# Optimization experiments

Measured on AMD Instinct MI355X. Metric: run time of the kernel, lower is better.

## Reference

```python
import jax, jax.numpy as jnp
import numpy as np


def setup_inputs() -> dict:
    key = jax.random.key(0)
    ka, kb = jax.random.split(key)
    a = jax.random.normal(ka, (8, 2048, 1024), dtype=jnp.float32)
    b = jax.random.normal(kb, (8, 2048, 1024), dtype=jnp.float32)
    return {"a": a, "b": b}


def reference(a, b):
    # e[b,i,j] = <a_i, b_j>
    e = jnp.einsum("bid,bjd->bij", a, b)  # [B, La, Lb]
    e_b = jax.nn.softmax(e, axis=2)        # softmax over b-tokens
    e_a = jax.nn.softmax(e, axis=1)        # softmax over a-tokens
    a_tilda = jnp.einsum("bij,bjd->bid", e_b, b)  # [B, La, D]
    b_tilda = jnp.einsum("bij,bid->bjd", e_a, a)  # [B, Lb, D]
    return (a_tilda, b_tilda)
```

## Files before the change

kernel.cpp:

```cpp
#include <hip/hip_runtime.h>

#define BATCH 8
#define L 2048
#define D 1024

#define PB_OFF  (L * L)
#define PAT_OFF (L * L + (L * L) / 2)
#define SLOT_F  (2 * L * L)

typedef __attribute__((ext_vector_type(8))) short bf16x8;
typedef __attribute__((ext_vector_type(4))) float f32x4;

static __device__ inline unsigned short f2bf(float x) {
  union { float f; unsigned u; } v; v.f = x;
  unsigned r = v.u + 0x7fff + ((v.u >> 16) & 1);
  return (unsigned short)(r >> 16);
}
static __device__ inline float bf2f(unsigned short h) {
  union { unsigned u; float f; } v; v.u = ((unsigned)h) << 16; return v.f;
}
static __device__ inline unsigned pack2(float x, float y) {
  return (unsigned)f2bf(x) | ((unsigned)f2bf(y) << 16);
}
static __device__ inline void split2(float x, float y, unsigned &hi, unsigned &lo) {
  unsigned short hx = f2bf(x), hy = f2bf(y);
  float rx = x - bf2f(hx), ry = y - bf2f(hy);
  hi = (unsigned)hx | ((unsigned)hy << 16);
  lo = (unsigned)f2bf(rx) | ((unsigned)f2bf(ry) << 16);
}

#define GLL16(gp, lp) __builtin_amdgcn_global_load_lds(                        \
    (const __attribute__((address_space(1))) void*)(gp),                       \
    (__attribute__((address_space(3))) void*)(lp), 16, 0, 0)

static __device__ inline void stage2(const unsigned short* __restrict__ g,
                                     size_t o0, size_t o1,
                                     unsigned short* l, int wb) {
  GLL16(g + o0, l + wb);
  GLL16(g + o1, l + wb + 2048);
}

__global__ __launch_bounds__(256) void k_prep(const float* __restrict__ A,
                                              const float* __restrict__ Bm,
                                              unsigned short* __restrict__ at,
                                              unsigned short* __restrict__ bt,
                                              unsigned short* __restrict__ ah,
                                              unsigned short* __restrict__ al,
                                              unsigned short* __restrict__ bh,
                                              unsigned short* __restrict__ bl) {
  const int z = blockIdx.z, batch = z & 7;
  const bool isA = z < 8;
  const float* src = (isA ? A : Bm) + (size_t)batch * L * D;
  unsigned short* dst = (isA ? at : bt) + (size_t)batch * D * L;
  unsigned short* ph = (isA ? ah : bh) + (size_t)batch * L * D;
  unsigned short* pl = (isA ? al : bl) + (size_t)batch * L * D;
  const int i0 = blockIdx.x * 64, d0 = blockIdx.y * 64;
  __shared__ float sT[64][65];
  const int tid = threadIdx.x;
#pragma unroll
  for (int it = 0; it < 4; ++it) {
    int idx = tid + it * 256;
    int row = idx >> 4, c4 = (idx & 15) * 4;
    float4 v = *(const float4*)(src + (size_t)(i0 + row) * D + d0 + c4);
    unsigned h0, l0, h1, l1;
    split2(v.x, v.y, h0, l0); split2(v.z, v.w, h1, l1);
    size_t po = (size_t)(i0 + row) * D + d0 + c4;
    *(uint2*)&ph[po] = make_uint2(h0, h1);
    *(uint2*)&pl[po] = make_uint2(l0, l1);
    sT[row][c4 + 0] = v.x; sT[row][c4 + 1] = v.y;
    sT[row][c4 + 2] = v.z; sT[row][c4 + 3] = v.w;
  }
  __syncthreads();
#pragma unroll
  for (int it = 0; it < 4; ++it) {
    int idx = tid + it * 256;
    int orow = idx >> 4, c4 = (idx & 15) * 4;
    uint2 o = make_uint2(pack2(sT[c4 + 0][orow], sT[c4 + 1][orow]),
                         pack2(sT[c4 + 2][orow], sT[c4 + 3][orow]));
    *(uint2*)&dst[(size_t)(d0 + orow) * L + i0 + c4] = o;
  }
}

__global__ __launch_bounds__(256) void k_gemm_e(const unsigned short* __restrict__ ah,
                                                const unsigned short* __restrict__ al,
                                                const unsigned short* __restrict__ bh,
                                                const unsigned short* __restrict__ bl,
                                                float* __restrict__ ws, int b0) {
  const int bz = blockIdx.z, batch = b0 + bz;
  const size_t po = (size_t)batch * L * D;
  float* e = ws + (size_t)bz * SLOT_F;
  const int i0 = blockIdx.x * 128, j0 = blockIdx.y * 128;
  __shared__ unsigned short sAh[128 * 32], sAl[128 * 32];
  __shared__ unsigned short sBh[128 * 32], sBl[128 * 32];
  const int tid = threadIdx.x, lane = tid & 63, wave = tid >> 6;
  const int wm = (wave & 1) * 64, wn = (wave >> 1) * 64;
  const int q = lane >> 4, lr = lane & 15;
  const int soff = wave * 1024 + lane * 16;
  const int srow = soff >> 6, scol = (soff & 63) >> 1;
  const int wb = wave * 512;
  const unsigned short* gAh = ah + po; const unsigned short* gAl = al + po;
  const unsigned short* gBh = bh + po; const unsigned short* gBl = bl + po;
  const size_t ga0 = (size_t)(i0 + srow) * D + scol, ga1 = ga0 + (size_t)64 * D;
  const size_t gb0 = (size_t)(j0 + srow) * D + scol, gb1 = gb0 + (size_t)64 * D;
  f32x4 acc[4][4] = {};
  for (int k0 = 0; k0 < D; k0 += 32) {
    __syncthreads();
    stage2(gAh, ga0 + k0, ga1 + k0, sAh, wb);
    stage2(gAl, ga0 + k0, ga1 + k0, sAl, wb);
    stage2(gBh, gb0 + k0, gb1 + k0, sBh, wb);
    stage2(gBl, gb0 + k0, gb1 + k0, sBl, wb);
    __syncthreads();
    bf16x8 fah[4], fbh[4], fx[4];
#pragma unroll
    for (int t = 0; t < 4; ++t) {
      fah[t] = *(const bf16x8*)&sAh[(wm + t * 16 + lr) * 32 + q * 8];
      fbh[t] = *(const bf16x8*)&sBh[(wn + t * 16 + lr) * 32 + q * 8];
    }
#pragma unroll
    for (int mi = 0; mi < 4; ++mi)
#pragma unroll
      for (int ni = 0; ni < 4; ++ni)
        acc[mi][ni] = __builtin_amdgcn_mfma_f32_16x16x32_bf16(fah[mi], fbh[ni], acc[mi][ni], 0, 0, 0);
#pragma unroll
    for (int t = 0; t < 4; ++t)
      fx[t] = *(const bf16x8*)&sBl[(wn + t * 16 + lr) * 32 + q * 8];
#pragma unroll
    for (int mi = 0; mi < 4; ++mi)
#pragma unroll
      for (int ni = 0; ni < 4; ++ni)
        acc[mi][ni] = __builtin_amdgcn_mfma_f32_16x16x32_bf16(fah[mi], fx[ni], acc[mi][ni], 0, 0, 0);
#pragma unroll
    for (int t = 0; t < 4; ++t)
      fx[t] = *(const bf16x8*)&sAl[(wm + t * 16 + lr) * 32 + q * 8];
#pragma unroll
    for (int mi = 0; mi < 4; ++mi)
#pragma unroll
      for (int ni = 0; ni < 4; ++ni)
        acc[mi][ni] = __builtin_amdgcn_mfma_f32_16x16x32_bf16(fx[mi], fbh[ni], acc[mi][ni], 0, 0, 0);
  }
#pragma unroll
  for (int mi = 0; mi < 4; ++mi)
#pragma unroll
    for (int ni = 0; ni < 4; ++ni)
#pragma unroll
      for (int r = 0; r < 4; ++r)
        e[(size_t)(i0 + wm + mi * 16 + q * 4 + r) * L + (j0 + wn + ni * 16 + lr)] =
            acc[mi][ni][r];
}

__global__ __launch_bounds__(256) void k_rowsoft(float* __restrict__ ws) {
  float* slot = ws + (size_t)blockIdx.y * SLOT_F;
  const int row = blockIdx.x, tid = threadIdx.x;
  const float* er = slot + (size_t)row * L;
  float v[8]; float m = -INFINITY;
#pragma unroll
  for (int r = 0; r < 8; ++r) { v[r] = er[tid + r * 256]; m = fmaxf(m, v[r]); }
  __shared__ float red[4];
#pragma unroll
  for (int o = 32; o; o >>= 1) m = fmaxf(m, __shfl_xor(m, o));
  if ((tid & 63) == 0) red[tid >> 6] = m;
  __syncthreads();
  m = fmaxf(fmaxf(red[0], red[1]), fmaxf(red[2], red[3]));
  float ex[8], s = 0.f;
#pragma unroll
  for (int r = 0; r < 8; ++r) { ex[r] = __expf(v[r] - m); s += ex[r]; }
  __syncthreads();
#pragma unroll
  for (int o = 32; o; o >>= 1) s += __shfl_xor(s, o);
  if ((tid & 63) == 0) red[tid >> 6] = s;
  __syncthreads();
  const float inv = 1.0f / (red[0] + red[1] + red[2] + red[3]);
  unsigned short* P = (unsigned short*)(slot + PB_OFF) + (size_t)row * L;
#pragma unroll
  for (int r = 0; r < 8; ++r) P[tid + r * 256] = f2bf(ex[r] * inv);
}

__global__ __launch_bounds__(512) void k_colsoft(float* __restrict__ ws) {
  float* slot = ws + (size_t)blockIdx.y * SLOT_F;
  const int j0 = blockIdx.x * 64;
  const int tid = threadIdx.x;
  const int c = tid & 63, rq = tid >> 6;
  const float* e = slot;
  const float* ec = e + j0 + c;
  float m = -INFINITY;
#pragma unroll 8
  for (int i = rq; i < L; i += 8) m = fmaxf(m, ec[(size_t)i * L]);
  __shared__ float red[8][64];
  red[rq][c] = m;
  __syncthreads();
#pragma unroll
  for (int k = 0; k < 8; ++k) m = fmaxf(m, red[k][c]);
  float s = 0.f;
#pragma unroll 8
  for (int i = rq; i < L; i += 8) s += __expf(ec[(size_t)i * L] - m);
  __syncthreads();
  red[rq][c] = s;
  __syncthreads();
  s = 0.f;
#pragma unroll
  for (int k = 0; k < 8; ++k) s += red[k][c];
  const float inv = 1.0f / s;
  __shared__ float scm[64], sci[64];
  if (rq == 0) { scm[c] = m; sci[c] = inv; }
  __shared__ unsigned short sT[64][72];
  unsigned short* PaT = (unsigned short*)(slot + PAT_OFF);
  for (int ii0 = 0; ii0 < L; ii0 += 64) {
    __syncthreads();
#pragma unroll
    for (int p = 0; p < 2; ++p) {
      int idx = tid + p * 512;
      int r = idx >> 4, c4 = (idx & 15) * 4;
      float4 v = *(const float4*)(e + (size_t)(ii0 + r) * L + j0 + c4);
      sT[c4 + 0][r] = f2bf(__expf(v.x - scm[c4 + 0]) * sci[c4 + 0]);
      sT[c4 + 1][r] = f2bf(__expf(v.y - scm[c4 + 1]) * sci[c4 + 1]);
      sT[c4 + 2][r] = f2bf(__expf(v.z - scm[c4 + 2]) * sci[c4 + 2]);
      sT[c4 + 3][r] = f2bf(__expf(v.w - scm[c4 + 3]) * sci[c4 + 3]);
    }
    __syncthreads();
    {
      int cc = tid >> 3, r8 = (tid & 7) * 8;
      uint4 o = *(const uint4*)&sT[cc][r8];
      *(uint4*)&PaT[(size_t)(j0 + cc) * L + ii0 + r8] = o;
    }
  }
}

__global__ __launch_bounds__(256) void k_pv(const unsigned short* __restrict__ Wt,
                                            const float* __restrict__ ws, int pOff,
                                            float* __restrict__ outB, int b0) {
  const int bz = blockIdx.z, batch = b0 + bz;
  const unsigned short* P = (const unsigned short*)(ws + (size_t)bz * SLOT_F + pOff);
  const unsigned short* W = Wt + (size_t)batch * D * L;
  const int m0 = blockIdx.x * 128, d0 = blockIdx.y * 128;
  __shared__ unsigned short sP[128 * 32], sW[128 * 32];
  const int tid = threadIdx.x, lane = tid & 63, wave = tid >> 6;
  const int wm = (wave & 1) * 64, wn = (wave >> 1) * 64;
  const int q = lane >> 4, lr = lane & 15;
  const int soff = wave * 1024 + lane * 16;
  const int srow = soff >> 6, scol = (soff & 63) >> 1;
  const int wb = wave * 512;
  const size_t gp0 = (size_t)(m0 + srow) * L + scol, gp1 = gp0 + (size_t)64 * L;
  const size_t gw0 = (size_t)(d0 + srow) * L + scol, gw1 = gw0 + (size_t)64 * L;
  f32x4 acc[4][4] = {};
  for (int k0 = 0; k0 < L; k0 += 32) {
    __syncthreads();
    stage2(P, gp0 + k0, gp1 + k0, sP, wb);
    stage2(W, gw0 + k0, gw1 + k0, sW, wb);
    __syncthreads();
    bf16x8 fa[4], fb[4];
#pragma unroll
    for (int t = 0; t < 4; ++t) {
      fa[t] = *(const bf16x8*)&sP[(wm + t * 16 + lr) * 32 + q * 8];
      fb[t] = *(const bf16x8*)&sW[(wn + t * 16 + lr) * 32 + q * 8];
    }
#pragma unroll
    for (int mi = 0; mi < 4; ++mi)
#pragma unroll
      for (int ni = 0; ni < 4; ++ni)
        acc[mi][ni] = __builtin_amdgcn_mfma_f32_16x16x32_bf16(fa[mi], fb[ni], acc[mi][ni], 0, 0, 0);
  }
  float* o = outB + (size_t)batch * L * D;
#pragma unroll
  for (int mi = 0; mi < 4; ++mi)
#pragma unroll
    for (int ni = 0; ni < 4; ++ni)
#pragma unroll
      for (int r = 0; r < 4; ++r)
        o[(size_t)(m0 + wm + mi * 16 + q * 4 + r) * D + (d0 + wn + ni * 16 + lr)] =
            acc[mi][ni][r];
}

extern "C" void kernel_launch(void* const* d_in, const int* in_sizes, int n_in,
                              void* d_out, int out_size, void* d_ws, size_t ws_size,
                              hipStream_t stream) {
  const float* a = (const float*)d_in[0];
  const float* b = (const float*)d_in[1];
  float* out = (float*)d_out;
  const size_t PL = (size_t)BATCH * D * L;
  unsigned short* at = (unsigned short*)d_ws;
  unsigned short* bt = at + PL;
  unsigned short* ah = bt + PL;
  unsigned short* al = ah + PL;
  unsigned short* bh = al + PL;
  unsigned short* bl = bh + PL;
  float* slots = (float*)(bl + PL);
  const size_t base_bytes = 6 * PL * sizeof(unsigned short);
  const size_t slot_bytes = (size_t)SLOT_F * sizeof(float);
  int S = 1;
  if (ws_size > base_bytes + slot_bytes)
    S = (int)((ws_size - base_bytes) / slot_bytes);
  if (S > BATCH) S = BATCH;
  if (S < 1) S = 1;

  hipLaunchKernelGGL(k_prep, dim3(L / 64, D / 64, 2 * BATCH), dim3(256), 0, stream,
                     a, b, at, bt, ah, al, bh, bl);
  for (int b0 = 0; b0 < BATCH; b0 += S) {
    int nb = (BATCH - b0 < S) ? (BATCH - b0) : S;
    hipLaunchKernelGGL(k_gemm_e, dim3(16, 16, nb), dim3(256), 0, stream,
                       ah, al, bh, bl, slots, b0);
    hipLaunchKernelGGL(k_rowsoft, dim3(L, nb), dim3(256), 0, stream, slots);
    hipLaunchKernelGGL(k_colsoft, dim3(L / 64, nb), dim3(512), 0, stream, slots);
    hipLaunchKernelGGL(k_pv, dim3(16, 8, nb), dim3(256), 0, stream,
                       bt, slots, PB_OFF, out, b0);
    hipLaunchKernelGGL(k_pv, dim3(16, 8, nb), dim3(256), 0, stream,
                       at, slots, PAT_OFF, out + (size_t)BATCH * L * D, b0);
  }
}
```

Baseline: 811.0 us.

## Fuse column-max into QK GEMM, split colsoftmax, defer normalization, merge PV launches

The QK GEMM epilogue now computes per-tile column maxima, so the column softmax no longer needs a separate max pass over E. Column work is split into small stat kernels plus a parallel exp/transposition kernel that also emits partial sums. Normalization by row and column reciprocal sums is deferred to the PV epilogue. The two PV launches are merged into one grid, with a 64-wide K tile, swizzled LDS and a GLL16 direct-load path. This adds more launches and extra stat buffers in the workspace.

Measured after the change: 738.3 us. -9.0%, faster.

```diff
diff --git a/kernel.cpp b/kernel.cpp
--- a/kernel.cpp
+++ b/kernel.cpp
@@ -6,7 +6,13 @@
 
 #define PB_OFF  (L * L)
 #define PAT_OFF (L * L + (L * L) / 2)
-#define SLOT_F  (2 * L * L)
+#define STAT    (2 * L * L)
+#define ROWINV  0
+#define CMAXP   (L)
+#define CMAX    (17 * L)
+#define CSUMP   (18 * L)
+#define CINV    (26 * L)
+#define SLOT_F  (2 * L * L + 28 * L)
 
 typedef __attribute__((ext_vector_type(8))) short bf16x8;
 typedef __attribute__((ext_vector_type(4))) float f32x4;
@@ -92,6 +98,7 @@
   const int i0 = blockIdx.x * 128, j0 = blockIdx.y * 128;
   __shared__ unsigned short sAh[128 * 32], sAl[128 * 32];
   __shared__ unsigned short sBh[128 * 32], sBl[128 * 32];
+  __shared__ float pcm[128];
   const int tid = threadIdx.x, lane = tid & 63, wave = tid >> 6;
   const int wm = (wave & 1) * 64, wn = (wave >> 1) * 64;
   const int q = lane >> 4, lr = lane & 15;
@@ -146,6 +153,29 @@
       for (int r = 0; r < 4; ++r)
         e[(size_t)(i0 + wm + mi * 16 + q * 4 + r) * L + (j0 + wn + ni * 16 + lr)] =
             acc[mi][ni][r];
+  float cmax[4];
+#pragma unroll
+  for (int ni = 0; ni < 4; ++ni) {
+    float m = acc[0][ni][0];
+#pragma unroll
+    for (int mi = 0; mi < 4; ++mi)
+#pragma unroll
+      for (int r = 0; r < 4; ++r) m = fmaxf(m, acc[mi][ni][r]);
+    m = fmaxf(m, __shfl_xor(m, 16));
+    m = fmaxf(m, __shfl_xor(m, 32));
+    cmax[ni] = m;
+  }
+  if (!(wave & 1) && q == 0)
+#pragma unroll
+    for (int ni = 0; ni < 4; ++ni) pcm[wn + ni * 16 + lr] = cmax[ni];
+  __syncthreads();
+  if ((wave & 1) && q == 0) {
+#pragma unroll
+    for (int ni = 0; ni < 4; ++ni) {
+      int c = wn + ni * 16 + lr;
+      e[STAT + CMAXP + (size_t)(i0 >> 7) * L + j0 + c] = fmaxf(cmax[ni], pcm[c]);
+    }
+  }
 }
 
 __global__ __launch_bounds__(256) void k_rowsoft(float* __restrict__ ws) {
@@ -169,105 +199,139 @@
   for (int o = 32; o; o >>= 1) s += __shfl_xor(s, o);
   if ((tid & 63) == 0) red[tid >> 6] = s;
   __syncthreads();
-  const float inv = 1.0f / (red[0] + red[1] + red[2] + red[3]);
   unsigned short* P = (unsigned short*)(slot + PB_OFF) + (size_t)row * L;
 #pragma unroll
-  for (int r = 0; r < 8; ++r) P[tid + r * 256] = f2bf(ex[r] * inv);
-}
-
-__global__ __launch_bounds__(512) void k_colsoft(float* __restrict__ ws) {
-  float* slot = ws + (size_t)blockIdx.y * SLOT_F;
-  const int j0 = blockIdx.x * 64;
+  for (int r = 0; r < 8; ++r) P[tid + r * 256] = f2bf(ex[r]);
+  if (tid == 0)
+    slot[STAT + ROWINV + row] = 1.0f / (red[0] + red[1] + red[2] + red[3]);
+}
+
+__global__ __launch_bounds__(256) void k_colstat2(float* __restrict__ ws) {
+  float* st = ws + (size_t)blockIdx.y * SLOT_F + STAT;
+  const int j = blockIdx.x * 256 + threadIdx.x;
+  float m = st[CMAXP + j];
+#pragma unroll
+  for (int k = 1; k < 16; ++k) m = fmaxf(m, st[CMAXP + (size_t)k * L + j]);
+  st[CMAX + j] = m;
+}
+
+__global__ __launch_bounds__(256) void k_colexp(float* __restrict__ ws) {
+  float* slot = ws + (size_t)blockIdx.z * SLOT_F;
+  const float* e = slot;
+  float* st = slot + STAT;
+  const int j0 = blockIdx.x * 64, i0 = blockIdx.y * 256;
   const int tid = threadIdx.x;
-  const int c = tid & 63, rq = tid >> 6;
-  const float* e = slot;
-  const float* ec = e + j0 + c;
-  float m = -INFINITY;
-#pragma unroll 8
-  for (int i = rq; i < L; i += 8) m = fmaxf(m, ec[(size_t)i * L]);
-  __shared__ float red[8][64];
-  red[rq][c] = m;
-  __syncthreads();
-#pragma unroll
-  for (int k = 0; k < 8; ++k) m = fmaxf(m, red[k][c]);
+  const int rr = tid >> 4, c4 = (tid & 15) * 4;
+  __shared__ unsigned short sT[64][72];
+  __shared__ float psumL[16][64];
+  float cm[4], ps[4] = {0.f, 0.f, 0.f, 0.f};
+#pragma unroll
+  for (int k = 0; k < 4; ++k) cm[k] = st[CMAX + j0 + c4 + k];
+  unsigned short* PaT = (unsigned short*)(slot + PAT_OFF);
+  for (int sub = 0; sub < 4; ++sub) {
+    const int ib = i0 + sub * 64;
+    __syncthreads();
+#pragma unroll
+    for (int p = 0; p < 4; ++p) {
+      const int r = rr + p * 16;
+      float4 v = *(const float4*)(e + (size_t)(ib + r) * L + j0 + c4);
+      float e0 = __expf(v.x - cm[0]), e1 = __expf(v.y - cm[1]);
+      float e2 = __expf(v.z - cm[2]), e3 = __expf(v.w - cm[3]);
+      ps[0] += e0; ps[1] += e1; ps[2] += e2; ps[3] += e3;
+      sT[c4 + 0][r] = f2bf(e0); sT[c4 + 1][r] = f2bf(e1);
+      sT[c4 + 2][r] = f2bf(e2); sT[c4 + 3][r] = f2bf(e3);
+    }
+    __syncthreads();
+    const int cc = tid >> 2, qd = tid & 3;
+    uint4 o0 = *(const uint4*)&sT[cc][qd * 8];
+    uint4 o1 = *(const uint4*)&sT[cc][32 + qd * 8];
+    *(uint4*)&PaT[(size_t)(j0 + cc) * L + ib + qd * 8] = o0;
+    *(uint4*)&PaT[(size_t)(j0 + cc) * L + ib + 32 + qd * 8] = o1;
+  }
+  psumL[rr][c4 + 0] = ps[0]; psumL[rr][c4 + 1] = ps[1];
+  psumL[rr][c4 + 2] = ps[2]; psumL[rr][c4 + 3] = ps[3];
+  __syncthreads();
+  if (tid < 64) {
+    float s = 0.f;
+#pragma unroll
+    for (int g = 0; g < 16; ++g) s += psumL[g][tid];
+    st[CSUMP + (size_t)blockIdx.y * L + j0 + tid] = s;
+  }
+}
+
+__global__ __launch_bounds__(256) void k_colfin(float* __restrict__ ws) {
+  float* st = ws + (size_t)blockIdx.y * SLOT_F + STAT;
+  const int j = blockIdx.x * 256 + threadIdx.x;
   float s = 0.f;
-#pragma unroll 8
-  for (int i = rq; i < L; i += 8) s += __expf(ec[(size_t)i * L] - m);
-  __syncthreads();
-  red[rq][c] = s;
-  __syncthreads();
-  s = 0.f;
-#pragma unroll
-  for (int k = 0; k < 8; ++k) s += red[k][c];
-  const float inv = 1.0f / s;
-  __shared__ float scm[64], sci[64];
-  if (rq == 0) { scm[c] = m; sci[c] = inv; }
-  __shared__ unsigned short sT[64][72];
-  unsigned short* PaT = (unsigned short*)(slot + PAT_OFF);
-  for (int ii0 = 0; ii0 < L; ii0 += 64) {
-    __syncthreads();
-#pragma unroll
-    for (int p = 0; p < 2; ++p) {
-      int idx = tid + p * 512;
-      int r = idx >> 4, c4 = (idx & 15) * 4;
-      float4 v = *(const float4*)(e + (size_t)(ii0 + r) * L + j0 + c4);
-      sT[c4 + 0][r] = f2bf(__expf(v.x - scm[c4 + 0]) * sci[c4 + 0]);
-      sT[c4 + 1][r] = f2bf(__expf(v.y - scm[c4 + 1]) * sci[c4 + 1]);
-      sT[c4 + 2][r] = f2bf(__expf(v.z - scm[c4 + 2]) * sci[c4 + 2]);
-      sT[c4 + 3][r] = f2bf(__expf(v.w - scm[c4 + 3]) * sci[c4 + 3]);
-    }
-    __syncthreads();
-    {
-      int cc = tid >> 3, r8 = (tid & 7) * 8;
-      uint4 o = *(const uint4*)&sT[cc][r8];
-      *(uint4*)&PaT[(size_t)(j0 + cc) * L + ii0 + r8] = o;
-    }
-  }
-}
-
-__global__ __launch_bounds__(256) void k_pv(const unsigned short* __restrict__ Wt,
-                                            const float* __restrict__ ws, int pOff,
-                                            float* __restrict__ outB, int b0) {
-  const int bz = blockIdx.z, batch = b0 + bz;
-  const unsigned short* P = (const unsigned short*)(ws + (size_t)bz * SLOT_F + pOff);
-  const unsigned short* W = Wt + (size_t)batch * D * L;
+#pragma unroll
+  for (int k = 0; k < 8; ++k) s += st[CSUMP + (size_t)k * L + j];
+  st[CINV + j] = 1.0f / s;
+}
+
+__global__ __launch_bounds__(256) void k_pv(const unsigned short* __restrict__ at,
+                                            const unsigned short* __restrict__ bt,
+                                            float* __restrict__ ws,
+                                            float* __restrict__ outB,
+                                            int b0, int nb) {
+  const int z = blockIdx.z;
+  const int pair = (z >= nb) ? 1 : 0;
+  const int bz = z - pair * nb;
+  const int batch = b0 + bz;
+  float* slot = ws + (size_t)bz * SLOT_F;
+  const unsigned short* P =
+      (const unsigned short*)(slot + (pair ? PAT_OFF : PB_OFF));
+  const unsigned short* W = (pair ? at : bt) + (size_t)batch * D * L;
+  float* out = outB + (size_t)(pair * BATCH + batch) * L * D;
+  const float* sc = slot + STAT + (pair ? CINV : ROWINV);
   const int m0 = blockIdx.x * 128, d0 = blockIdx.y * 128;
-  __shared__ unsigned short sP[128 * 32], sW[128 * 32];
+  __shared__ unsigned short sP[128 * 64], sW[128 * 64];
   const int tid = threadIdx.x, lane = tid & 63, wave = tid >> 6;
   const int wm = (wave & 1) * 64, wn = (wave >> 1) * 64;
   const int q = lane >> 4, lr = lane & 15;
-  const int soff = wave * 1024 + lane * 16;
-  const int srow = soff >> 6, scol = (soff & 63) >> 1;
-  const int wb = wave * 512;
-  const size_t gp0 = (size_t)(m0 + srow) * L + scol, gp1 = gp0 + (size_t)64 * L;
-  const size_t gw0 = (size_t)(d0 + srow) * L + scol, gw1 = gw0 + (size_t)64 * L;
+  const int srow = wave * 8 + (lane >> 3);
+  const int scolu = ((lane & 7) ^ (lane >> 3)) * 8;
+  const size_t gp = (size_t)(m0 + srow) * L + scolu;
+  const size_t gw = (size_t)(d0 + srow) * L + scolu;
+  const int ldsb = wave * 512;
+  const int swz = (lr & 7) << 3;
   f32x4 acc[4][4] = {};
-  for (int k0 = 0; k0 < L; k0 += 32) {
-    __syncthreads();
-    stage2(P, gp0 + k0, gp1 + k0, sP, wb);
-    stage2(W, gw0 + k0, gw1 + k0, sW, wb);
-    __syncthreads();
-    bf16x8 fa[4], fb[4];
-#pragma unroll
-    for (int t = 0; t < 4; ++t) {
-      fa[t] = *(const bf16x8*)&sP[(wm + t * 16 + lr) * 32 + q * 8];
-      fb[t] = *(const bf16x8*)&sW[(wn + t * 16 + lr) * 32 + q * 8];
-    }
-#pragma unroll
-    for (int mi = 0; mi < 4; ++mi)
-#pragma unroll
-      for (int ni = 0; ni < 4; ++ni)
-        acc[mi][ni] = __builtin_amdgcn_mfma_f32_16x16x32_bf16(fa[mi], fb[ni], acc[mi][ni], 0, 0, 0);
-  }
-  float* o = outB + (size_t)batch * L * D;
+  for (int k0 = 0; k0 < L; k0 += 64) {
+    __syncthreads();
+#pragma unroll
+    for (int it = 0; it < 4; ++it) {
+      GLL16(P + gp + (size_t)it * 32 * L + k0, sP + ldsb + it * 2048);
+      GLL16(W + gw + (size_t)it * 32 * L + k0, sW + ldsb + it * 2048);
+    }
+    __syncthreads();
+#pragma unroll
+    for (int kk = 0; kk < 2; ++kk) {
+      bf16x8 fa[4], fb[4];
+#pragma unroll
+      for (int t = 0; t < 4; ++t) {
+        fa[t] = *(const bf16x8*)&sP[(wm + t * 16 + lr) * 64 + ((kk * 32 + q * 8) ^ swz)];
+        fb[t] = *(const bf16x8*)&sW[(wn + t * 16 + lr) * 64 + ((kk * 32 + q * 8) ^ swz)];
+      }
+#pragma unroll
+      for (int mi = 0; mi < 4; ++mi)
+#pragma unroll
+        for (int ni = 0; ni < 4; ++ni)
+          acc[mi][ni] = __builtin_amdgcn_mfma_f32_16x16x32_bf16(fa[mi], fb[ni], acc[mi][ni], 0, 0, 0);
+    }
+  }
+  float rsc[4][4];
 #pragma unroll
   for (int mi = 0; mi < 4; ++mi)
 #pragma unroll
+    for (int r = 0; r < 4; ++r)
+      rsc[mi][r] = sc[m0 + wm + mi * 16 + q * 4 + r];
+#pragma unroll
+  for (int mi = 0; mi < 4; ++mi)
+#pragma unroll
     for (int ni = 0; ni < 4; ++ni)
 #pragma unroll
       for (int r = 0; r < 4; ++r)
-        o[(size_t)(m0 + wm + mi * 16 + q * 4 + r) * D + (d0 + wn + ni * 16 + lr)] =
-            acc[mi][ni][r];
+        out[(size_t)(m0 + wm + mi * 16 + q * 4 + r) * D + (d0 + wn + ni * 16 + lr)] =
+            acc[mi][ni][r] * rsc[mi][r];
 }
 
 extern "C" void kernel_launch(void* const* d_in, const int* in_sizes, int n_in,
@@ -299,10 +363,10 @@
     hipLaunchKernelGGL(k_gemm_e, dim3(16, 16, nb), dim3(256), 0, stream,
                        ah, al, bh, bl, slots, b0);
     hipLaunchKernelGGL(k_rowsoft, dim3(L, nb), dim3(256), 0, stream, slots);
-    hipLaunchKernelGGL(k_colsoft, dim3(L / 64, nb), dim3(512), 0, stream, slots);
-    hipLaunchKernelGGL(k_pv, dim3(16, 8, nb), dim3(256), 0, stream,
-                       bt, slots, PB_OFF, out, b0);
-    hipLaunchKernelGGL(k_pv, dim3(16, 8, nb), dim3(256), 0, stream,
-                       at, slots, PAT_OFF, out + (size_t)BATCH * L * D, b0);
-  }
-}
+    hipLaunchKernelGGL(k_colstat2, dim3(L / 256, nb), dim3(256), 0, stream, slots);
+    hipLaunchKernelGGL(k_colexp, dim3(L / 64, L / 256, nb), dim3(256), 0, stream, slots);
+    hipLaunchKernelGGL(k_colfin, dim3(L / 256, nb), dim3(256), 0, stream, slots);
+    hipLaunchKernelGGL(k_pv, dim3(16, 8, 2 * nb), dim3(256), 0, stream,
+                       at, bt, slots, out, b0, nb);
+  }
+}
```
